# Kernel optimization log

Hardware: AMD Instinct MI355X
Metric: run time of the kernel (lower is better)

## Reference

```python
import jax, jax.numpy as jnp
import numpy as np

EPSILON = 1e-8
DT = 0.1
STEPS = 3
MASK_DENSITY = 0.01


def setup_inputs() -> dict:
    key = jax.random.key(0)
    k1, k2 = jax.random.split(key)
    B, S, D = 4, 4096, 2
    psi = jax.random.normal(k1, (B, S, D), dtype=jnp.float32)
    # binary mask: threshold a uniform draw to get a sparse 0/1 adjacency
    u = jax.random.uniform(k2, (B, S, S), dtype=jnp.float32)
    binary_mask = (u < MASK_DENSITY).astype(jnp.float32)
    return {"psi": psi, "binary_mask": binary_mask}


def reference(psi, binary_mask):
    def force(state):
        # adjacency-weighted aggregation minus self: [B,S,S] @ [B,S,2]
        return jnp.einsum('bij,bjd->bid', binary_mask, state) - state

    def step(p, _):
        r = jnp.linalg.norm(p, axis=-1, keepdims=True)          # [B,S,1]
        k1 = force(p)
        psi_star = p + DT * k1
        star_norm = jnp.linalg.norm(psi_star, axis=-1, keepdims=True)
        psi_star = psi_star * (r / (star_norm + EPSILON))       # renormalize to r
        k2 = force(psi_star)
        p_new = p + 0.5 * DT * (k1 + k2)
        new_norm = jnp.linalg.norm(p_new, axis=-1, keepdims=True)
        p_new = p_new * (r / (new_norm + EPSILON))              # norm-preserving
        return p_new, None

    psi_out, _ = jax.lax.scan(step, psi, None, length=STEPS)
    return psi_out
```

## Files before the change

kernel.cpp:

```cpp
#include <hip/hip_runtime.h>
#include <stdint.h>

#define BATCH   4
#define SEQ     4096
#define NROWS   (BATCH * SEQ)
#define MAXC    128
#define DTS     0.1f
#define HALF_DT 0.05f
#define EPS     1e-8f

__global__ __launch_bounds__(256)
void compress_phaseA(const float* __restrict__ mask,
                     const float2* __restrict__ psi,
                     unsigned short* __restrict__ csr,
                     int*   __restrict__ cnts,
                     float2* __restrict__ k1buf,
                     float2* __restrict__ starbuf,
                     float*  __restrict__ rbuf) {
    const int row  = (blockIdx.x * blockDim.x + threadIdx.x) >> 6;
    const int lane = threadIdx.x & 63;
    const float4* src = reinterpret_cast<const float4*>(mask + (size_t)row * SEQ);

    float4 d[16];
#pragma unroll
    for (int c = 0; c < 16; ++c) d[c] = src[c * 64 + lane];

    int n = 0;
#pragma unroll
    for (int c = 0; c < 16; ++c)
        n += (d[c].x != 0.f) + (d[c].y != 0.f) + (d[c].z != 0.f) + (d[c].w != 0.f);

    int inc = n;
#pragma unroll
    for (int dd = 1; dd < 64; dd <<= 1) {
        int t = __shfl_up(inc, dd, 64);
        if (lane >= dd) inc += t;
    }
    int excl  = inc - n;
    int total = __shfl(inc, 63, 64);
    if (lane == 0) cnts[row] = (total < MAXC) ? total : MAXC;

    const int bidx = row >> 12;
    const float2* gb = psi + ((size_t)bidx << 12);
    unsigned short* dst = csr + (size_t)row * MAXC;
    int k = excl;
    float sx = 0.f, sy = 0.f;
    const int cb = lane << 2;
#pragma unroll
    for (int c = 0; c < 16; ++c) {
        const int col = c * 256 + cb;
        if (d[c].x != 0.f) { if (k < MAXC) dst[k] = (unsigned short)(col + 0); ++k;
                             float2 s = gb[col + 0]; sx += s.x; sy += s.y; }
        if (d[c].y != 0.f) { if (k < MAXC) dst[k] = (unsigned short)(col + 1); ++k;
                             float2 s = gb[col + 1]; sx += s.x; sy += s.y; }
        if (d[c].z != 0.f) { if (k < MAXC) dst[k] = (unsigned short)(col + 2); ++k;
                             float2 s = gb[col + 2]; sx += s.x; sy += s.y; }
        if (d[c].w != 0.f) { if (k < MAXC) dst[k] = (unsigned short)(col + 3); ++k;
                             float2 s = gb[col + 3]; sx += s.x; sy += s.y; }
    }
#pragma unroll
    for (int m = 32; m >= 1; m >>= 1) {
        sx += __shfl_xor(sx, m, 64);
        sy += __shfl_xor(sy, m, 64);
    }

    float2 p  = psi[row];
    float r   = sqrtf(p.x * p.x + p.y * p.y);
    float k1x = sx - p.x, k1y = sy - p.y;
    float tx  = p.x + DTS * k1x, ty = p.y + DTS * k1y;
    float sc  = r / (sqrtf(tx * tx + ty * ty) + EPS);
    if (lane == 0) {
        k1buf[row]   = make_float2(k1x, k1y);
        starbuf[row] = make_float2(tx * sc, ty * sc);
        rbuf[row]    = r;
    }
}

template <int PHASE>
__global__ __launch_bounds__(256)
void force_step(const unsigned short* __restrict__ csr,
                const int*   __restrict__ cnts,
                const float2* __restrict__ pIn,
                const float2* __restrict__ gsrc,
                float2* __restrict__ k1buf,
                float2* __restrict__ starbuf,
                float*  __restrict__ rbuf,
                float2* __restrict__ outbuf) {
    const int row  = (blockIdx.x * blockDim.x + threadIdx.x) >> 6;
    const int lane = threadIdx.x & 63;
    const int bidx = row >> 12;
    const float2* gb = gsrc + ((size_t)bidx << 12);
    const unsigned short* cs = csr + (size_t)row * MAXC;

    const int cnt = cnts[row];
    float sx = 0.f, sy = 0.f;
    for (int base = 0; base < cnt; base += 64) {
        const int i = base + lane;
        if (i < cnt) {
            float2 v = gb[cs[i]];
            sx += v.x; sy += v.y;
        }
    }
#pragma unroll
    for (int m = 32; m >= 1; m >>= 1) {
        sx += __shfl_xor(sx, m, 64);
        sy += __shfl_xor(sy, m, 64);
    }

    if (lane == 0) {
        if (PHASE == 0) {
            float2 p = pIn[row];
            float r   = sqrtf(p.x * p.x + p.y * p.y);
            float k1x = sx - p.x, k1y = sy - p.y;
            float tx  = p.x + DTS * k1x, ty = p.y + DTS * k1y;
            float sc  = r / (sqrtf(tx * tx + ty * ty) + EPS);
            k1buf[row]   = make_float2(k1x, k1y);
            starbuf[row] = make_float2(tx * sc, ty * sc);
            rbuf[row]    = r;
        } else {
            float2 st = gsrc[row];
            float k2x = sx - st.x, k2y = sy - st.y;
            float2 p  = pIn[row];
            float2 k1 = k1buf[row];
            float nx  = p.x + HALF_DT * (k1.x + k2x);
            float ny  = p.y + HALF_DT * (k1.y + k2y);
            float sc  = rbuf[row] / (sqrtf(nx * nx + ny * ny) + EPS);
            outbuf[row] = make_float2(nx * sc, ny * sc);
        }
    }
}

extern "C" void kernel_launch(void* const* d_in, const int* in_sizes, int n_in,
                              void* d_out, int out_size, void* d_ws, size_t ws_size,
                              hipStream_t stream) {
    const float* psi  = (const float*)d_in[0];
    const float* mask = (const float*)d_in[1];
    float2* out2 = (float2*)d_out;

    char* ws = (char*)d_ws;
    float2* p    = (float2*)ws;
    float2* k1   = p + NROWS;
    float2* star = k1 + NROWS;
    float*  rbuf = (float*)(star + NROWS);
    int*    cnts = (int*)(rbuf + NROWS);
    unsigned short* csr = (unsigned short*)(cnts + NROWS);

    const float2* psi2 = (const float2*)psi;
    const int grid = NROWS / 4;

    compress_phaseA<<<grid, 256, 0, stream>>>(mask, psi2, csr, cnts, k1, star, rbuf);
    force_step<1><<<grid, 256, 0, stream>>>(csr, cnts, psi2, star, k1, star, rbuf, p);
    force_step<0><<<grid, 256, 0, stream>>>(csr, cnts, p, p, k1, star, rbuf, nullptr);
    force_step<1><<<grid, 256, 0, stream>>>(csr, cnts, p, star, k1, star, rbuf, p);
    force_step<0><<<grid, 256, 0, stream>>>(csr, cnts, p, p, k1, star, rbuf, nullptr);
    force_step<1><<<grid, 256, 0, stream>>>(csr, cnts, p, star, k1, star, rbuf, out2);
}
```

Baseline: 398.7 us.

## Fuse all integration steps into one per-batch kernel with LDS-resident state

The mask compression kernel now only builds the CSR column lists and counts; it no longer gathers psi for the first force. The five force_step launches are replaced by one integrate kernel with one 1024-thread block per batch. That block keeps psi and psi_star in shared memory, holds k1 and r in registers, and reads CSR indices as uint4 vectors. MAXC is also reduced to 96 to shrink the CSR buffer. This removes launch overhead and global round-trips for intermediate buffers, but runs the whole sparse integration on only four workgroups, so it depends on the LDS gathers being latency-tolerant.

```diff
diff --git a/kernel.cpp b/kernel.cpp
--- a/kernel.cpp
+++ b/kernel.cpp
@@ -4,19 +4,15 @@
 #define BATCH   4
 #define SEQ     4096
 #define NROWS   (BATCH * SEQ)
-#define MAXC    128
+#define MAXC    96
 #define DTS     0.1f
 #define HALF_DT 0.05f
 #define EPS     1e-8f
 
 __global__ __launch_bounds__(256)
-void compress_phaseA(const float* __restrict__ mask,
-                     const float2* __restrict__ psi,
-                     unsigned short* __restrict__ csr,
-                     int*   __restrict__ cnts,
-                     float2* __restrict__ k1buf,
-                     float2* __restrict__ starbuf,
-                     float*  __restrict__ rbuf) {
+void compress_csr(const float* __restrict__ mask,
+                  unsigned short* __restrict__ csr,
+                  int* __restrict__ cnts) {
     const int row  = (blockIdx.x * blockDim.x + threadIdx.x) >> 6;
     const int lane = threadIdx.x & 63;
     const float4* src = reinterpret_cast<const float4*>(mask + (size_t)row * SEQ);
@@ -40,93 +36,99 @@
     int total = __shfl(inc, 63, 64);
     if (lane == 0) cnts[row] = (total < MAXC) ? total : MAXC;
 
-    const int bidx = row >> 12;
-    const float2* gb = psi + ((size_t)bidx << 12);
     unsigned short* dst = csr + (size_t)row * MAXC;
     int k = excl;
-    float sx = 0.f, sy = 0.f;
     const int cb = lane << 2;
 #pragma unroll
     for (int c = 0; c < 16; ++c) {
         const int col = c * 256 + cb;
-        if (d[c].x != 0.f) { if (k < MAXC) dst[k] = (unsigned short)(col + 0); ++k;
-                             float2 s = gb[col + 0]; sx += s.x; sy += s.y; }
-        if (d[c].y != 0.f) { if (k < MAXC) dst[k] = (unsigned short)(col + 1); ++k;
-                             float2 s = gb[col + 1]; sx += s.x; sy += s.y; }
-        if (d[c].z != 0.f) { if (k < MAXC) dst[k] = (unsigned short)(col + 2); ++k;
-                             float2 s = gb[col + 2]; sx += s.x; sy += s.y; }
-        if (d[c].w != 0.f) { if (k < MAXC) dst[k] = (unsigned short)(col + 3); ++k;
-                             float2 s = gb[col + 3]; sx += s.x; sy += s.y; }
-    }
-#pragma unroll
-    for (int m = 32; m >= 1; m >>= 1) {
-        sx += __shfl_xor(sx, m, 64);
-        sy += __shfl_xor(sy, m, 64);
-    }
-
-    float2 p  = psi[row];
-    float r   = sqrtf(p.x * p.x + p.y * p.y);
-    float k1x = sx - p.x, k1y = sy - p.y;
-    float tx  = p.x + DTS * k1x, ty = p.y + DTS * k1y;
-    float sc  = r / (sqrtf(tx * tx + ty * ty) + EPS);
-    if (lane == 0) {
-        k1buf[row]   = make_float2(k1x, k1y);
-        starbuf[row] = make_float2(tx * sc, ty * sc);
-        rbuf[row]    = r;
+        if (d[c].x != 0.f) { if (k < MAXC) dst[k] = (unsigned short)(col + 0); ++k; }
+        if (d[c].y != 0.f) { if (k < MAXC) dst[k] = (unsigned short)(col + 1); ++k; }
+        if (d[c].z != 0.f) { if (k < MAXC) dst[k] = (unsigned short)(col + 2); ++k; }
+        if (d[c].w != 0.f) { if (k < MAXC) dst[k] = (unsigned short)(col + 3); ++k; }
     }
 }
 
-template <int PHASE>
-__global__ __launch_bounds__(256)
-void force_step(const unsigned short* __restrict__ csr,
-                const int*   __restrict__ cnts,
-                const float2* __restrict__ pIn,
-                const float2* __restrict__ gsrc,
-                float2* __restrict__ k1buf,
-                float2* __restrict__ starbuf,
-                float*  __restrict__ rbuf,
-                float2* __restrict__ outbuf) {
-    const int row  = (blockIdx.x * blockDim.x + threadIdx.x) >> 6;
-    const int lane = threadIdx.x & 63;
-    const int bidx = row >> 12;
-    const float2* gb = gsrc + ((size_t)bidx << 12);
-    const unsigned short* cs = csr + (size_t)row * MAXC;
-
-    const int cnt = cnts[row];
-    float sx = 0.f, sy = 0.f;
-    for (int base = 0; base < cnt; base += 64) {
-        const int i = base + lane;
-        if (i < cnt) {
-            float2 v = gb[cs[i]];
+__device__ __forceinline__ void gather8(const float2* __restrict__ lds,
+                                        uint4 q, int base, int cnt,
+                                        float& sx, float& sy) {
+    unsigned id[8] = { q.x & 0xffffu, q.x >> 16, q.y & 0xffffu, q.y >> 16,
+                       q.z & 0xffffu, q.z >> 16, q.w & 0xffffu, q.w >> 16 };
+#pragma unroll
+    for (int e = 0; e < 8; ++e) {
+        if (base + e < cnt) {
+            float2 v = lds[id[e]];
             sx += v.x; sy += v.y;
         }
     }
+}
+
+__device__ __forceinline__ float2 row_sum(const unsigned short* __restrict__ cs,
+                                          int cnt, const float2* __restrict__ lds) {
+    const uint4* cv = reinterpret_cast<const uint4*>(cs);
+    float sx = 0.f, sy = 0.f;
+    for (int c = 0; c * 8 < cnt; ++c)
+        gather8(lds, cv[c], c * 8, cnt, sx, sy);
+    return make_float2(sx, sy);
+}
+
+__global__ __launch_bounds__(1024, 1)
+void integrate(const unsigned short* __restrict__ csr,
+               const int* __restrict__ cnts,
+               const float2* __restrict__ psi,
+               float2* __restrict__ out) {
+    __shared__ float2 pl[SEQ];
+    __shared__ float2 sl[SEQ];
+    const int b = blockIdx.x;
+    const int t = threadIdx.x;
+    const int rbase = b << 12;
+
+    int cnt[4];
+    const float2* pb = psi + ((size_t)b << 12);
 #pragma unroll
-    for (int m = 32; m >= 1; m >>= 1) {
-        sx += __shfl_xor(sx, m, 64);
-        sy += __shfl_xor(sy, m, 64);
+    for (int j = 0; j < 4; ++j) {
+        const int row = j * 1024 + t;
+        pl[row] = pb[row];
+        cnt[j]  = cnts[rbase + row];
     }
+    __syncthreads();
 
-    if (lane == 0) {
-        if (PHASE == 0) {
-            float2 p = pIn[row];
+    float2 k1r[4];
+    float  rr[4];
+
+    for (int s = 0; s < 3; ++s) {
+#pragma unroll
+        for (int j = 0; j < 4; ++j) {
+            const int row = j * 1024 + t;
+            const unsigned short* cs = csr + (size_t)(rbase + row) * MAXC;
+            float2 sum = row_sum(cs, cnt[j], pl);
+            float2 p  = pl[row];
             float r   = sqrtf(p.x * p.x + p.y * p.y);
-            float k1x = sx - p.x, k1y = sy - p.y;
+            float k1x = sum.x - p.x, k1y = sum.y - p.y;
             float tx  = p.x + DTS * k1x, ty = p.y + DTS * k1y;
             float sc  = r / (sqrtf(tx * tx + ty * ty) + EPS);
-            k1buf[row]   = make_float2(k1x, k1y);
-            starbuf[row] = make_float2(tx * sc, ty * sc);
-            rbuf[row]    = r;
-        } else {
-            float2 st = gsrc[row];
-            float k2x = sx - st.x, k2y = sy - st.y;
-            float2 p  = pIn[row];
-            float2 k1 = k1buf[row];
-            float nx  = p.x + HALF_DT * (k1.x + k2x);
-            float ny  = p.y + HALF_DT * (k1.y + k2y);
-            float sc  = rbuf[row] / (sqrtf(nx * nx + ny * ny) + EPS);
-            outbuf[row] = make_float2(nx * sc, ny * sc);
+            k1r[j] = make_float2(k1x, k1y);
+            rr[j]  = r;
+            sl[row] = make_float2(tx * sc, ty * sc);
         }
+        __syncthreads();
+
+#pragma unroll
+        for (int j = 0; j < 4; ++j) {
+            const int row = j * 1024 + t;
+            const unsigned short* cs = csr + (size_t)(rbase + row) * MAXC;
+            float2 sum = row_sum(cs, cnt[j], sl);
+            float2 st = sl[row];
+            float2 p  = pl[row];
+            float k2x = sum.x - st.x, k2y = sum.y - st.y;
+            float nx  = p.x + HALF_DT * (k1r[j].x + k2x);
+            float ny  = p.y + HALF_DT * (k1r[j].y + k2y);
+            float sc  = rr[j] / (sqrtf(nx * nx + ny * ny) + EPS);
+            float2 pn = make_float2(nx * sc, ny * sc);
+            if (s == 2) out[rbase + row] = pn;
+            else        pl[row] = pn;
+        }
+        __syncthreads();
     }
 }
 
@@ -138,20 +140,11 @@
     float2* out2 = (float2*)d_out;
 
     char* ws = (char*)d_ws;
-    float2* p    = (float2*)ws;
-    float2* k1   = p + NROWS;
-    float2* star = k1 + NROWS;
-    float*  rbuf = (float*)(star + NROWS);
-    int*    cnts = (int*)(rbuf + NROWS);
+    int* cnts = (int*)ws;
     unsigned short* csr = (unsigned short*)(cnts + NROWS);
 
     const float2* psi2 = (const float2*)psi;
-    const int grid = NROWS / 4;
 
-    compress_phaseA<<<grid, 256, 0, stream>>>(mask, psi2, csr, cnts, k1, star, rbuf);
-    force_step<1><<<grid, 256, 0, stream>>>(csr, cnts, psi2, star, k1, star, rbuf, p);
-    force_step<0><<<grid, 256, 0, stream>>>(csr, cnts, p, p, k1, star, rbuf, nullptr);
-    force_step<1><<<grid, 256, 0, stream>>>(csr, cnts, p, star, k1, star, rbuf, p);
-    force_step<0><<<grid, 256, 0, stream>>>(csr, cnts, p, p, k1, star, rbuf, nullptr);
-    force_step<1><<<grid, 256, 0, stream>>>(csr, cnts, p, star, k1, star, rbuf, out2);
+    compress_csr<<<NROWS / 4, 256, 0, stream>>>(mask, csr, cnts);
+    integrate<<<BATCH, 1024, 0, stream>>>(csr, cnts, psi2, out2);
 }
```

Measured after the change: 482.3 us. 1.21x slower.
